# Performance work log

Measured on AMD Instinct MI355X. Metric: run time of the kernel, lower is better.

## Reference

```python
import jax, jax.numpy as jnp
import numpy as np

N, E, G = 20000, 50000, 64          # nodes, edges, graphs
IN_DIM, EDGE_DIM, H, OUT_DIM = 32, 16, 64, 6
EPS = 1e-5  # BatchNorm eps


def setup_inputs() -> dict:
    key = jax.random.key(0)
    ks = jax.random.split(key, 24)
    s = 0.05
    inp = {
        "x": jax.random.normal(ks[0], (N, IN_DIM), jnp.float32),
        "edge_attr": jax.random.normal(ks[1], (E, EDGE_DIM), jnp.float32),
        "src": jax.random.randint(ks[2], (E,), 0, N, jnp.int32),
        "dst": jax.random.randint(ks[3], (E,), 0, N, jnp.int32),
        "batch": jnp.sort(jax.random.randint(ks[4], (N,), 0, G, jnp.int32)),
        # node encoder
        "Wx": jax.random.normal(ks[5], (IN_DIM, H), jnp.float32) * s,
        "bx": jnp.zeros((H,), jnp.float32),
        # three edge MLPs: edge_dim -> H*H
        "We": jax.random.normal(ks[6], (3, EDGE_DIM, H * H), jnp.float32) * s,
        "be": jnp.zeros((3, H * H), jnp.float32),
        # NNConv root weights / biases
        "Wroot": jax.random.normal(ks[7], (3, H, H), jnp.float32) * s,
        "broot": jnp.zeros((3, H), jnp.float32),
        # BatchNorm (eval mode: running stats)
        "gamma": jnp.ones((3, H), jnp.float32),
        "beta": jnp.zeros((3, H), jnp.float32),
        "run_mean": jnp.zeros((3, H), jnp.float32),
        "run_var": jnp.ones((3, H), jnp.float32),
        # head
        "W1": jax.random.normal(ks[8], (H, H), jnp.float32) * s,
        "b1": jnp.zeros((H,), jnp.float32),
        "W2": jax.random.normal(ks[9], (H, OUT_DIM), jnp.float32) * s,
        "b2": jnp.zeros((OUT_DIM,), jnp.float32),
    }
    return inp


def _segment_mean(vals, idx, num_segments):
    tot = jax.ops.segment_sum(vals, idx, num_segments=num_segments)
    cnt = jax.ops.segment_sum(jnp.ones((vals.shape[0],), vals.dtype), idx,
                              num_segments=num_segments)
    return tot / jnp.maximum(cnt, 1.0)[:, None]


def reference(x, edge_attr, src, dst, batch, Wx, bx, We, be, Wroot, broot,
              gamma, beta, run_mean, run_var, W1, b1, W2, b2):
    h = x @ Wx + bx                                      # (N, H)
    for l in range(3):
        # per-edge H x H weight matrices from the edge MLP
        ew = jax.nn.relu(edge_attr @ We[l] + be[l]).reshape(-1, H, H)  # (E, H, H)
        msg = jnp.einsum('eh,eho->eo', h[src], ew)       # gather + per-edge matvec
        agg = _segment_mean(msg, dst, N)                 # scatter-mean at destinations
        out = agg + h @ Wroot[l] + broot[l]              # NNConv root + bias
        out = jax.nn.relu(out)
        # BatchNorm1d in eval mode (running stats); dropout is identity in eval
        out = gamma[l] * (out - run_mean[l]) * jax.lax.rsqrt(run_var[l] + EPS) + beta[l]
        h = out + h                                      # residual (shapes always match)
    pooled = _segment_mean(h, batch, G)                  # global_mean_pool -> (G, H)
    z = jax.nn.relu(pooled @ W1 + b1)
    return z @ W2 + b2                                   # (G, OUT_DIM)
```

## Files before the change

kernel.cpp:

```cpp
#include <hip/hip_runtime.h>
#include <hip/hip_bf16.h>

typedef _Float16 f16x2 __attribute__((ext_vector_type(2)));
typedef _Float16 f16x8 __attribute__((ext_vector_type(8)));
typedef float    f32x16 __attribute__((ext_vector_type(16)));

#define IN_DIM   32
#define EDGE_DIM 16
#define HDIM     64
#define OUT_DIM  6
#define BN_EPS   1e-5f

__global__ void k_zero(uint4* __restrict__ p, int n16) {
    int i = blockIdx.x * 256 + threadIdx.x;
    if (i < n16) p[i] = make_uint4(0u, 0u, 0u, 0u);
}

__global__ __launch_bounds__(256) void k_setup(
    const float* __restrict__ We, uint4* __restrict__ WeB,
    const float* __restrict__ x, const float* __restrict__ Wx,
    const float* __restrict__ bx, float* __restrict__ h,
    const float* __restrict__ ea, _Float16* __restrict__ eaH,
    const int* __restrict__ dstI, int* __restrict__ degI,
    const int* __restrict__ batch, int* __restrict__ start,
    int N, int E, int G, int PACKB, int ENCB, int PREPB)
{
    int bid = blockIdx.x;
    int t = threadIdx.x;
    if (bid < PACKB) {
        int tid = bid * 256 + t;
        int tile = tid >> 6, lane = tid & 63;
        int layer = tile >> 7;
        int r = tile & 127;
        int hh = r >> 1, oh = r & 1;
        int col = hh * 64 + oh * 32 + (lane & 31);
        int kbase = 8 * (lane >> 5);
        const float* base = We + (size_t)layer * 65536 + col;
        f16x8 v;
        #pragma unroll
        for (int j = 0; j < 8; ++j) v[j] = (_Float16)base[(size_t)(kbase + j) * 4096];
        WeB[(size_t)tile * 64 + lane] = __builtin_bit_cast(uint4, v);
        return;
    }
    bid -= PACKB;
    if (bid < ENCB) {
        int tid = bid * 256 + t;
        int n = tid >> 4, jq = tid & 15;
        if (n >= N) return;
        const float4* W4 = (const float4*)Wx;
        float4 acc = ((const float4*)bx)[jq];
        const float4* xv = (const float4*)(x + (size_t)n * IN_DIM);
        #pragma unroll
        for (int k4 = 0; k4 < 8; ++k4) {
            float4 xk = xv[k4];
            #pragma unroll
            for (int i = 0; i < 4; ++i) {
                float xs = (i == 0) ? xk.x : (i == 1) ? xk.y : (i == 2) ? xk.z : xk.w;
                float4 ww = W4[(k4 * 4 + i) * 16 + jq];
                acc.x += xs * ww.x; acc.y += xs * ww.y; acc.z += xs * ww.z; acc.w += xs * ww.w;
            }
        }
        ((float4*)h)[tid] = acc;
        return;
    }
    bid -= ENCB;
    if (bid < PREPB) {
        int tid = bid * 256 + t;
        int E8 = E * 8;
        if (tid < E8) {
            float2 v = ((const float2*)ea)[tid];
            f16x2 r; r[0] = (_Float16)v.x; r[1] = (_Float16)v.y;
            ((f16x2*)eaH)[tid] = r;
        }
        if (tid < E) atomicAdd(&degI[dstI[tid]], 1);
        return;
    }
    if (t <= G) {
        int lo = 0, hi = N;
        while (lo < hi) { int mid = (lo + hi) >> 1; if (batch[mid] < t) lo = mid + 1; else hi = mid; }
        start[t] = lo;
    }
}

__global__ __launch_bounds__(256, 4) void k_edge(
    const uint4* __restrict__ eaH4, const uint4* __restrict__ WeB,
    const float* __restrict__ be, const float* __restrict__ hin,
    const int* __restrict__ srcI, const int* __restrict__ dstI,
    float* __restrict__ agg, int E)
{
    __shared__ __align__(16) float hsT[64][68];
    __shared__ float beL[4096];
    const int t = threadIdx.x;
    const int l = t & 63;
    const int w = t >> 6;
    const int eb = blockIdx.x * 64;
    {
        const float4* bg = (const float4*)be;
        float4* bs = (float4*)beL;
        for (int i = t; i < 1024; i += 256) bs[i] = bg[i];
    }
    {
        int egc = min(eb + l, E - 1);
        int s = srcI[egc];
        const float4* hp = (const float4*)(hin + (size_t)s * HDIM + w * 16);
        float4 a = hp[0], b = hp[1], c = hp[2], d = hp[3];
        hsT[w*16+ 0][l] = a.x; hsT[w*16+ 1][l] = a.y; hsT[w*16+ 2][l] = a.z; hsT[w*16+ 3][l] = a.w;
        hsT[w*16+ 4][l] = b.x; hsT[w*16+ 5][l] = b.y; hsT[w*16+ 6][l] = b.z; hsT[w*16+ 7][l] = b.w;
        hsT[w*16+ 8][l] = c.x; hsT[w*16+ 9][l] = c.y; hsT[w*16+10][l] = c.z; hsT[w*16+11][l] = c.w;
        hsT[w*16+12][l] = d.x; hsT[w*16+13][l] = d.y; hsT[w*16+14][l] = d.z; hsT[w*16+15][l] = d.w;
    }
    __syncthreads();
    const int gp = w >> 1, oh = w & 1;
    const int ebw = eb + gp * 32, elw = gp * 32;
    const int row = l & 31, kg = l >> 5, obase = oh * 32;
    int ea_e = min(ebw + row, E - 1);
    f16x8 A = __builtin_bit_cast(f16x8, eaH4[(size_t)ea_e * 2 + kg]);
    float m[16];
    #pragma unroll
    for (int j = 0; j < 16; ++j) m[j] = 0.f;
    const uint4* Bb = WeB + (size_t)oh * 64 + l;
    uint4 Bv = Bb[0];
    for (int hh = 0; hh < 64; ++hh) {
        uint4 Bn;
        if (hh < 63) Bn = Bb[(size_t)(hh + 1) * 128];
        float bias = beL[hh * 64 + obase + row];
        f32x16 cin;
        #pragma unroll
        for (int j = 0; j < 16; ++j) cin[j] = bias;
        f32x16 z = __builtin_amdgcn_mfma_f32_32x32x16_f16(A, __builtin_bit_cast(f16x8, Bv), cin, 0, 0, 0);
        float4 q0 = *(const float4*)&hsT[hh][elw + 4 * kg + 0];
        float4 q1 = *(const float4*)&hsT[hh][elw + 4 * kg + 8];
        float4 q2 = *(const float4*)&hsT[hh][elw + 4 * kg + 16];
        float4 q3 = *(const float4*)&hsT[hh][elw + 4 * kg + 24];
        m[0]+=fmaxf(z[0],0.f)*q0.x;  m[1]+=fmaxf(z[1],0.f)*q0.y;
        m[2]+=fmaxf(z[2],0.f)*q0.z;  m[3]+=fmaxf(z[3],0.f)*q0.w;
        m[4]+=fmaxf(z[4],0.f)*q1.x;  m[5]+=fmaxf(z[5],0.f)*q1.y;
        m[6]+=fmaxf(z[6],0.f)*q1.z;  m[7]+=fmaxf(z[7],0.f)*q1.w;
        m[8]+=fmaxf(z[8],0.f)*q2.x;  m[9]+=fmaxf(z[9],0.f)*q2.y;
        m[10]+=fmaxf(z[10],0.f)*q2.z; m[11]+=fmaxf(z[11],0.f)*q2.w;
        m[12]+=fmaxf(z[12],0.f)*q3.x; m[13]+=fmaxf(z[13],0.f)*q3.y;
        m[14]+=fmaxf(z[14],0.f)*q3.z; m[15]+=fmaxf(z[15],0.f)*q3.w;
        Bv = Bn;
    }
    #pragma unroll
    for (int j = 0; j < 16; ++j) {
        int e = ebw + (j & 3) + 8 * (j >> 2) + 4 * kg;
        if (e < E) atomicAdd(&agg[(size_t)dstI[e] * HDIM + obase + row], m[j]);
    }
}

__global__ void k_update(
    float* __restrict__ agg, const int* __restrict__ degI,
    const float* __restrict__ hin, const float* __restrict__ Wroot,
    const float* __restrict__ broot, const float* __restrict__ gam,
    const float* __restrict__ bet, const float* __restrict__ rmean,
    const float* __restrict__ rvar, float* __restrict__ hout, int N)
{
    int tid = blockIdx.x * 256 + threadIdx.x;
    int n = tid >> 4, jq = tid & 15;
    if (n >= N) return;
    float dinv = 1.0f / fmaxf((float)degI[n], 1.0f);
    float4 acc = ((const float4*)broot)[jq];
    float4 ag = ((const float4*)agg)[tid];
    ((float4*)agg)[tid] = make_float4(0.f, 0.f, 0.f, 0.f);
    acc.x += ag.x * dinv; acc.y += ag.y * dinv; acc.z += ag.z * dinv; acc.w += ag.w * dinv;
    const float4* W4 = (const float4*)Wroot;
    const float4* hv = (const float4*)(hin + (size_t)n * HDIM);
    #pragma unroll
    for (int k4 = 0; k4 < 16; ++k4) {
        float4 hk = hv[k4];
        #pragma unroll
        for (int i = 0; i < 4; ++i) {
            float hsc = (i == 0) ? hk.x : (i == 1) ? hk.y : (i == 2) ? hk.z : hk.w;
            float4 ww = W4[(k4 * 4 + i) * 16 + jq];
            acc.x += hsc * ww.x; acc.y += hsc * ww.y; acc.z += hsc * ww.z; acc.w += hsc * ww.w;
        }
    }
    acc.x = fmaxf(acc.x, 0.f); acc.y = fmaxf(acc.y, 0.f);
    acc.z = fmaxf(acc.z, 0.f); acc.w = fmaxf(acc.w, 0.f);
    float4 g4 = ((const float4*)gam)[jq];
    float4 b4 = ((const float4*)bet)[jq];
    float4 mm4 = ((const float4*)rmean)[jq];
    float4 v4 = ((const float4*)rvar)[jq];
    float4 hres = ((const float4*)hin)[tid];
    float4 y;
    y.x = g4.x * (acc.x - mm4.x) * rsqrtf(v4.x + BN_EPS) + b4.x + hres.x;
    y.y = g4.y * (acc.y - mm4.y) * rsqrtf(v4.y + BN_EPS) + b4.y + hres.y;
    y.z = g4.z * (acc.z - mm4.z) * rsqrtf(v4.z + BN_EPS) + b4.z + hres.z;
    y.w = g4.w * (acc.w - mm4.w) * rsqrtf(v4.w + BN_EPS) + b4.w + hres.w;
    ((float4*)hout)[tid] = y;
}

__global__ __launch_bounds__(256) void k_pool_head(
    const float* __restrict__ h, const int* __restrict__ start,
    const float* __restrict__ W1, const float* __restrict__ b1,
    const float* __restrict__ W2, const float* __restrict__ b2,
    float* __restrict__ out)
{
    __shared__ float sums[16][68];
    __shared__ float pl[HDIM];
    __shared__ float zl[HDIM];
    int g = blockIdx.x;
    int s0 = start[g], s1 = start[g + 1];
    int t = threadIdx.x, jq = t & 15, rp = t >> 4;
    float4 acc = make_float4(0.f, 0.f, 0.f, 0.f);
    for (int n = s0 + rp; n < s1; n += 16) {
        float4 v = ((const float4*)h)[(size_t)n * 16 + jq];
        acc.x += v.x; acc.y += v.y; acc.z += v.z; acc.w += v.w;
    }
    *(float4*)&sums[rp][jq * 4] = acc;
    __syncthreads();
    if (t < HDIM) {
        float a = 0.f;
        #pragma unroll
        for (int r = 0; r < 16; ++r) a += sums[r][t];
        pl[t] = a / fmaxf((float)(s1 - s0), 1.0f);
    }
    __syncthreads();
    if (t < HDIM) {
        float a = b1[t];
        #pragma unroll
        for (int k = 0; k < HDIM; ++k) a += pl[k] * W1[k * HDIM + t];
        zl[t] = fmaxf(a, 0.f);
    }
    __syncthreads();
    if (t < OUT_DIM) {
        float a = b2[t];
        #pragma unroll
        for (int k = 0; k < HDIM; ++k) a += zl[k] * W2[k * OUT_DIM + t];
        out[(size_t)g * OUT_DIM + t] = a;
    }
}

extern "C" void kernel_launch(void* const* d_in, const int* in_sizes, int n_in,
                              void* d_out, int out_size, void* d_ws, size_t ws_size,
                              hipStream_t stream) {
    const float* x     = (const float*)d_in[0];
    const float* eattr = (const float*)d_in[1];
    const int*   src   = (const int*)d_in[2];
    const int*   dst   = (const int*)d_in[3];
    const int*   batch = (const int*)d_in[4];
    const float* Wx    = (const float*)d_in[5];
    const float* bx    = (const float*)d_in[6];
    const float* We    = (const float*)d_in[7];
    const float* be    = (const float*)d_in[8];
    const float* Wroot = (const float*)d_in[9];
    const float* broot = (const float*)d_in[10];
    const float* gam   = (const float*)d_in[11];
    const float* bet   = (const float*)d_in[12];
    const float* rmean = (const float*)d_in[13];
    const float* rvar  = (const float*)d_in[14];
    const float* W1    = (const float*)d_in[15];
    const float* b1    = (const float*)d_in[16];
    const float* W2    = (const float*)d_in[17];
    const float* b2    = (const float*)d_in[18];
    float* out = (float*)d_out;

    const int N = in_sizes[0] / IN_DIM;
    const int E = in_sizes[2];
    const int G = out_size / OUT_DIM;

    char* ws = (char*)d_ws;
    size_t off = 0;
    auto alloc = [&](size_t bytes) -> void* {
        void* p = ws + off;
        off = (off + bytes + 255) & ~(size_t)255;
        return p;
    };
    float*    h0    = (float*)alloc((size_t)N * HDIM * 4);
    float*    h1    = (float*)alloc((size_t)N * HDIM * 4);
    _Float16* eaH   = (_Float16*)alloc((size_t)E * 16 * 2);
    uint4*    WeB   = (uint4*)alloc((size_t)3 * 128 * 64 * 16);
    int*      start = (int*)alloc((size_t)(G + 1) * 4);
    size_t zoff = off;
    float*    agg   = (float*)alloc((size_t)N * HDIM * 4);
    int*      degI  = (int*)alloc((size_t)N * 4);
    size_t zbytes = off - zoff;
    (void)ws_size; (void)n_in;

    const int n16 = (int)(zbytes / 16);
    k_zero<<<(n16 + 255) / 256, 256, 0, stream>>>((uint4*)agg, n16);

    const int PACKB = 96;
    const int ENCB  = (N * 16 + 255) / 256;
    const int PREPB = (E * 8 + 255) / 256;
    k_setup<<<PACKB + ENCB + PREPB + 1, 256, 0, stream>>>(
        We, WeB, x, Wx, bx, h0, eattr, eaH, dst, degI, batch, start,
        N, E, G, PACKB, ENCB, PREPB);

    const float* hin = h0;
    float* hout = h1;
    const int edgeBlocks = (E + 63) / 64;
    for (int l = 0; l < 3; ++l) {
        k_edge<<<edgeBlocks, 256, 0, stream>>>(
            (const uint4*)eaH, WeB + (size_t)l * 8192, be + (size_t)l * 4096,
            hin, src, dst, agg, E);
        k_update<<<(N * 16 + 255) / 256, 256, 0, stream>>>(
            agg, degI, hin, Wroot + (size_t)l * 4096, broot + (size_t)l * 64,
            gam + (size_t)l * 64, bet + (size_t)l * 64, rmean + (size_t)l * 64,
            rvar + (size_t)l * 64, hout, N);
        float* tmp = hout; hout = (float*)hin; hin = tmp;
    }
    k_pool_head<<<G, 256, 0, stream>>>(hin, start, W1, b1, W2, b2, out);
}
```

Measured before the change: 211.9 us.

## Split edge kernel over hidden-dim halves and read transposed bias from global

Each edge block now handles only half of the 64 input-hidden rows, which doubles the grid and halves the per-block shared tile. The 16 KB per-block shared copy of the edge-MLP bias is dropped. A transposed bias array is built once in the setup kernel and read as float4 directly from global memory, with the bias added after the MFMA instead of preloaded into the accumulator. The hidden loop is unrolled by four with B prefetch and the occupancy hint is raised. Splitting the work doubles the atomic scatter traffic to agg and the A/src loads, in exchange for less shared memory and higher occupancy.

```diff
diff --git a/kernel.cpp b/kernel.cpp
--- a/kernel.cpp
+++ b/kernel.cpp
@@ -18,6 +18,7 @@
 
 __global__ __launch_bounds__(256) void k_setup(
     const float* __restrict__ We, uint4* __restrict__ WeB,
+    const float* __restrict__ be, float* __restrict__ beT,
     const float* __restrict__ x, const float* __restrict__ Wx,
     const float* __restrict__ bx, float* __restrict__ h,
     const float* __restrict__ ea, _Float16* __restrict__ eaH,
@@ -43,6 +44,14 @@
         return;
     }
     bid -= PACKB;
+    if (bid < 3) {
+        int layer = bid;
+        for (int i = t; i < 4096; i += 256) {
+            beT[(size_t)layer * 4096 + (i & 63) * 64 + (i >> 6)] = be[(size_t)layer * 4096 + i];
+        }
+        return;
+    }
+    bid -= 3;
     if (bid < ENCB) {
         int tid = bid * 256 + t;
         int n = tid >> 4, jq = tid & 15;
@@ -82,34 +91,31 @@
     }
 }
 
-__global__ __launch_bounds__(256, 4) void k_edge(
+__global__ __launch_bounds__(256, 6) void k_edge(
     const uint4* __restrict__ eaH4, const uint4* __restrict__ WeB,
-    const float* __restrict__ be, const float* __restrict__ hin,
+    const float* __restrict__ beT, const float* __restrict__ hin,
     const int* __restrict__ srcI, const int* __restrict__ dstI,
     float* __restrict__ agg, int E)
 {
-    __shared__ __align__(16) float hsT[64][68];
-    __shared__ float beL[4096];
+    __shared__ __align__(16) float hsT[32][68];
     const int t = threadIdx.x;
     const int l = t & 63;
     const int w = t >> 6;
-    const int eb = blockIdx.x * 64;
-    {
-        const float4* bg = (const float4*)be;
-        float4* bs = (float4*)beL;
-        for (int i = t; i < 1024; i += 256) bs[i] = bg[i];
-    }
+    const int eg = blockIdx.x >> 1;
+    const int hhalf = blockIdx.x & 1;
+    const int eb = eg * 64;
+    const int hbase = hhalf * 32;
+
     {
         int egc = min(eb + l, E - 1);
         int s = srcI[egc];
-        const float4* hp = (const float4*)(hin + (size_t)s * HDIM + w * 16);
-        float4 a = hp[0], b = hp[1], c = hp[2], d = hp[3];
-        hsT[w*16+ 0][l] = a.x; hsT[w*16+ 1][l] = a.y; hsT[w*16+ 2][l] = a.z; hsT[w*16+ 3][l] = a.w;
-        hsT[w*16+ 4][l] = b.x; hsT[w*16+ 5][l] = b.y; hsT[w*16+ 6][l] = b.z; hsT[w*16+ 7][l] = b.w;
-        hsT[w*16+ 8][l] = c.x; hsT[w*16+ 9][l] = c.y; hsT[w*16+10][l] = c.z; hsT[w*16+11][l] = c.w;
-        hsT[w*16+12][l] = d.x; hsT[w*16+13][l] = d.y; hsT[w*16+14][l] = d.z; hsT[w*16+15][l] = d.w;
+        const float4* hp = (const float4*)(hin + (size_t)s * HDIM + hbase + w * 8);
+        float4 a = hp[0], b = hp[1];
+        hsT[w*8+0][l] = a.x; hsT[w*8+1][l] = a.y; hsT[w*8+2][l] = a.z; hsT[w*8+3][l] = a.w;
+        hsT[w*8+4][l] = b.x; hsT[w*8+5][l] = b.y; hsT[w*8+6][l] = b.z; hsT[w*8+7][l] = b.w;
     }
     __syncthreads();
+
     const int gp = w >> 1, oh = w & 1;
     const int ebw = eb + gp * 32, elw = gp * 32;
     const int row = l & 31, kg = l >> 5, obase = oh * 32;
@@ -118,30 +124,54 @@
     float m[16];
     #pragma unroll
     for (int j = 0; j < 16; ++j) m[j] = 0.f;
+
+    const f32x16 zc = (f32x16)0.f;
     const uint4* Bb = WeB + (size_t)oh * 64 + l;
-    uint4 Bv = Bb[0];
-    for (int hh = 0; hh < 64; ++hh) {
-        uint4 Bn;
-        if (hh < 63) Bn = Bb[(size_t)(hh + 1) * 128];
-        float bias = beL[hh * 64 + obase + row];
-        f32x16 cin;
-        #pragma unroll
-        for (int j = 0; j < 16; ++j) cin[j] = bias;
-        f32x16 z = __builtin_amdgcn_mfma_f32_32x32x16_f16(A, __builtin_bit_cast(f16x8, Bv), cin, 0, 0, 0);
+    const float* beTb = beT + (size_t)(obase + row) * 64 + hbase;
+
+    auto step = [&](const uint4& Bv, int hh, float bias) {
+        f32x16 z = __builtin_amdgcn_mfma_f32_32x32x16_f16(
+            A, __builtin_bit_cast(f16x8, Bv), zc, 0, 0, 0);
         float4 q0 = *(const float4*)&hsT[hh][elw + 4 * kg + 0];
         float4 q1 = *(const float4*)&hsT[hh][elw + 4 * kg + 8];
         float4 q2 = *(const float4*)&hsT[hh][elw + 4 * kg + 16];
         float4 q3 = *(const float4*)&hsT[hh][elw + 4 * kg + 24];
-        m[0]+=fmaxf(z[0],0.f)*q0.x;  m[1]+=fmaxf(z[1],0.f)*q0.y;
-        m[2]+=fmaxf(z[2],0.f)*q0.z;  m[3]+=fmaxf(z[3],0.f)*q0.w;
-        m[4]+=fmaxf(z[4],0.f)*q1.x;  m[5]+=fmaxf(z[5],0.f)*q1.y;
-        m[6]+=fmaxf(z[6],0.f)*q1.z;  m[7]+=fmaxf(z[7],0.f)*q1.w;
-        m[8]+=fmaxf(z[8],0.f)*q2.x;  m[9]+=fmaxf(z[9],0.f)*q2.y;
-        m[10]+=fmaxf(z[10],0.f)*q2.z; m[11]+=fmaxf(z[11],0.f)*q2.w;
-        m[12]+=fmaxf(z[12],0.f)*q3.x; m[13]+=fmaxf(z[13],0.f)*q3.y;
-        m[14]+=fmaxf(z[14],0.f)*q3.z; m[15]+=fmaxf(z[15],0.f)*q3.w;
-        Bv = Bn;
-    }
+        m[0]  += fmaxf(z[0]  + bias, 0.f) * q0.x;
+        m[1]  += fmaxf(z[1]  + bias, 0.f) * q0.y;
+        m[2]  += fmaxf(z[2]  + bias, 0.f) * q0.z;
+        m[3]  += fmaxf(z[3]  + bias, 0.f) * q0.w;
+        m[4]  += fmaxf(z[4]  + bias, 0.f) * q1.x;
+        m[5]  += fmaxf(z[5]  + bias, 0.f) * q1.y;
+        m[6]  += fmaxf(z[6]  + bias, 0.f) * q1.z;
+        m[7]  += fmaxf(z[7]  + bias, 0.f) * q1.w;
+        m[8]  += fmaxf(z[8]  + bias, 0.f) * q2.x;
+        m[9]  += fmaxf(z[9]  + bias, 0.f) * q2.y;
+        m[10] += fmaxf(z[10] + bias, 0.f) * q2.z;
+        m[11] += fmaxf(z[11] + bias, 0.f) * q2.w;
+        m[12] += fmaxf(z[12] + bias, 0.f) * q3.x;
+        m[13] += fmaxf(z[13] + bias, 0.f) * q3.y;
+        m[14] += fmaxf(z[14] + bias, 0.f) * q3.z;
+        m[15] += fmaxf(z[15] + bias, 0.f) * q3.w;
+    };
+
+    uint4 B0 = Bb[(size_t)(hbase + 0) * 128];
+    uint4 B1 = Bb[(size_t)(hbase + 1) * 128];
+    uint4 B2 = Bb[(size_t)(hbase + 2) * 128];
+    uint4 B3 = Bb[(size_t)(hbase + 3) * 128];
+    #pragma unroll 1
+    for (int hh = 0; hh < 32; hh += 4) {
+        uint4 N0 = Bb[(size_t)(hbase + hh + 4) * 128];
+        uint4 N1 = Bb[(size_t)(hbase + hh + 5) * 128];
+        uint4 N2 = Bb[(size_t)(hbase + hh + 6) * 128];
+        uint4 N3 = Bb[(size_t)(hbase + hh + 7) * 128];
+        float4 bv = *(const float4*)(beTb + hh);
+        step(B0, hh + 0, bv.x);
+        step(B1, hh + 1, bv.y);
+        step(B2, hh + 2, bv.z);
+        step(B3, hh + 3, bv.w);
+        B0 = N0; B1 = N1; B2 = N2; B3 = N3;
+    }
+
     #pragma unroll
     for (int j = 0; j < 16; ++j) {
         int e = ebw + (j & 3) + 8 * (j >> 2) + 4 * kg;
@@ -270,7 +300,8 @@
     float*    h0    = (float*)alloc((size_t)N * HDIM * 4);
     float*    h1    = (float*)alloc((size_t)N * HDIM * 4);
     _Float16* eaH   = (_Float16*)alloc((size_t)E * 16 * 2);
-    uint4*    WeB   = (uint4*)alloc((size_t)3 * 128 * 64 * 16);
+    uint4*    WeB   = (uint4*)alloc((size_t)3 * 128 * 64 * 16 + 65536);
+    float*    beT   = (float*)alloc((size_t)3 * 4096 * 4);
     int*      start = (int*)alloc((size_t)(G + 1) * 4);
     size_t zoff = off;
     float*    agg   = (float*)alloc((size_t)N * HDIM * 4);
@@ -284,16 +315,16 @@
     const int PACKB = 96;
     const int ENCB  = (N * 16 + 255) / 256;
     const int PREPB = (E * 8 + 255) / 256;
-    k_setup<<<PACKB + ENCB + PREPB + 1, 256, 0, stream>>>(
-        We, WeB, x, Wx, bx, h0, eattr, eaH, dst, degI, batch, start,
+    k_setup<<<PACKB + 3 + ENCB + PREPB + 1, 256, 0, stream>>>(
+        We, WeB, be, beT, x, Wx, bx, h0, eattr, eaH, dst, degI, batch, start,
         N, E, G, PACKB, ENCB, PREPB);
 
     const float* hin = h0;
     float* hout = h1;
-    const int edgeBlocks = (E + 63) / 64;
+    const int edgeBlocks = ((E + 63) / 64) * 2;
     for (int l = 0; l < 3; ++l) {
         k_edge<<<edgeBlocks, 256, 0, stream>>>(
-            (const uint4*)eaH, WeB + (size_t)l * 8192, be + (size_t)l * 4096,
+            (const uint4*)eaH, WeB + (size_t)l * 8192, beT + (size_t)l * 4096,
             hin, src, dst, agg, E);
         k_update<<<(N * 16 + 255) / 256, 256, 0, stream>>>(
             agg, degI, hin, Wroot + (size_t)l * 4096, broot + (size_t)l * 64,
```

New measurement: 500.3 us. +136.1%, slower.

## Stream edge-MLP weights into LDS ring via async global_load_lds pipeline

Applied to the files above, without the earlier changes.

Replaces the register-prefetched per-iteration weight load in the edge kernel with a 4-slot per-wave LDS ring filled by asynchronous global-to-LDS loads, issued three iterations ahead and guarded by explicit vmcnt waits. The bias is now added after the MFMA instead of being broadcast into the accumulator input, and occupancy hint drops from 4 to 3 blocks per CU because of the extra LDS. The aim is to hide global weight-load latency behind MFMA work. In exchange it relies on manual waitcnt correctness, adds LDS traffic, and may reduce occupancy.

```diff
diff --git a/kernel.cpp b/kernel.cpp
--- a/kernel.cpp
+++ b/kernel.cpp
@@ -10,6 +10,9 @@
 #define HDIM     64
 #define OUT_DIM  6
 #define BN_EPS   1e-5f
+
+typedef __attribute__((address_space(1))) const void GASV;
+typedef __attribute__((address_space(3))) void LASV;
 
 __global__ void k_zero(uint4* __restrict__ p, int n16) {
     int i = blockIdx.x * 256 + threadIdx.x;
@@ -82,7 +85,7 @@
     }
 }
 
-__global__ __launch_bounds__(256, 4) void k_edge(
+__global__ __launch_bounds__(256, 3) void k_edge(
     const uint4* __restrict__ eaH4, const uint4* __restrict__ WeB,
     const float* __restrict__ be, const float* __restrict__ hin,
     const int* __restrict__ srcI, const int* __restrict__ dstI,
@@ -90,10 +93,12 @@
 {
     __shared__ __align__(16) float hsT[64][68];
     __shared__ float beL[4096];
+    __shared__ __align__(16) uint4 Bring[4][4][64];
     const int t = threadIdx.x;
     const int l = t & 63;
     const int w = t >> 6;
     const int eb = blockIdx.x * 64;
+
     {
         const float4* bg = (const float4*)be;
         float4* bs = (float4*)beL;
@@ -109,39 +114,58 @@
         hsT[w*16+ 8][l] = c.x; hsT[w*16+ 9][l] = c.y; hsT[w*16+10][l] = c.z; hsT[w*16+11][l] = c.w;
         hsT[w*16+12][l] = d.x; hsT[w*16+13][l] = d.y; hsT[w*16+14][l] = d.z; hsT[w*16+15][l] = d.w;
     }
-    __syncthreads();
     const int gp = w >> 1, oh = w & 1;
     const int ebw = eb + gp * 32, elw = gp * 32;
     const int row = l & 31, kg = l >> 5, obase = oh * 32;
+
+    const uint4* gsrc = WeB + (size_t)oh * 64 + l;
+    #pragma unroll
+    for (int s = 0; s < 3; ++s) {
+        __builtin_amdgcn_global_load_lds((GASV*)(gsrc + (size_t)s * 128),
+                                         (LASV*)&Bring[w][s][0], 16, 0, 0);
+    }
+    __syncthreads();
+
     int ea_e = min(ebw + row, E - 1);
     f16x8 A = __builtin_bit_cast(f16x8, eaH4[(size_t)ea_e * 2 + kg]);
     float m[16];
     #pragma unroll
     for (int j = 0; j < 16; ++j) m[j] = 0.f;
-    const uint4* Bb = WeB + (size_t)oh * 64 + l;
-    uint4 Bv = Bb[0];
+    const f32x16 zc = (f32x16)0.f;
+
+    #pragma unroll 1
     for (int hh = 0; hh < 64; ++hh) {
-        uint4 Bn;
-        if (hh < 63) Bn = Bb[(size_t)(hh + 1) * 128];
+        asm volatile("s_waitcnt vmcnt(2)" ::: "memory");
+        __builtin_amdgcn_sched_barrier(0);
+        uint4 Bv = Bring[w][hh & 3][l];
         float bias = beL[hh * 64 + obase + row];
-        f32x16 cin;
-        #pragma unroll
-        for (int j = 0; j < 16; ++j) cin[j] = bias;
-        f32x16 z = __builtin_amdgcn_mfma_f32_32x32x16_f16(A, __builtin_bit_cast(f16x8, Bv), cin, 0, 0, 0);
+        f32x16 z = __builtin_amdgcn_mfma_f32_32x32x16_f16(
+            A, __builtin_bit_cast(f16x8, Bv), zc, 0, 0, 0);
+        int hn = (hh + 3) & 63;
+        __builtin_amdgcn_global_load_lds((GASV*)(gsrc + (size_t)hn * 128),
+                                         (LASV*)&Bring[w][hn & 3][0], 16, 0, 0);
         float4 q0 = *(const float4*)&hsT[hh][elw + 4 * kg + 0];
         float4 q1 = *(const float4*)&hsT[hh][elw + 4 * kg + 8];
         float4 q2 = *(const float4*)&hsT[hh][elw + 4 * kg + 16];
         float4 q3 = *(const float4*)&hsT[hh][elw + 4 * kg + 24];
-        m[0]+=fmaxf(z[0],0.f)*q0.x;  m[1]+=fmaxf(z[1],0.f)*q0.y;
-        m[2]+=fmaxf(z[2],0.f)*q0.z;  m[3]+=fmaxf(z[3],0.f)*q0.w;
-        m[4]+=fmaxf(z[4],0.f)*q1.x;  m[5]+=fmaxf(z[5],0.f)*q1.y;
-        m[6]+=fmaxf(z[6],0.f)*q1.z;  m[7]+=fmaxf(z[7],0.f)*q1.w;
-        m[8]+=fmaxf(z[8],0.f)*q2.x;  m[9]+=fmaxf(z[9],0.f)*q2.y;
-        m[10]+=fmaxf(z[10],0.f)*q2.z; m[11]+=fmaxf(z[11],0.f)*q2.w;
-        m[12]+=fmaxf(z[12],0.f)*q3.x; m[13]+=fmaxf(z[13],0.f)*q3.y;
-        m[14]+=fmaxf(z[14],0.f)*q3.z; m[15]+=fmaxf(z[15],0.f)*q3.w;
-        Bv = Bn;
-    }
+        m[0]  += fmaxf(z[0]  + bias, 0.f) * q0.x;
+        m[1]  += fmaxf(z[1]  + bias, 0.f) * q0.y;
+        m[2]  += fmaxf(z[2]  + bias, 0.f) * q0.z;
+        m[3]  += fmaxf(z[3]  + bias, 0.f) * q0.w;
+        m[4]  += fmaxf(z[4]  + bias, 0.f) * q1.x;
+        m[5]  += fmaxf(z[5]  + bias, 0.f) * q1.y;
+        m[6]  += fmaxf(z[6]  + bias, 0.f) * q1.z;
+        m[7]  += fmaxf(z[7]  + bias, 0.f) * q1.w;
+        m[8]  += fmaxf(z[8]  + bias, 0.f) * q2.x;
+        m[9]  += fmaxf(z[9]  + bias, 0.f) * q2.y;
+        m[10] += fmaxf(z[10] + bias, 0.f) * q2.z;
+        m[11] += fmaxf(z[11] + bias, 0.f) * q2.w;
+        m[12] += fmaxf(z[12] + bias, 0.f) * q3.x;
+        m[13] += fmaxf(z[13] + bias, 0.f) * q3.y;
+        m[14] += fmaxf(z[14] + bias, 0.f) * q3.z;
+        m[15] += fmaxf(z[15] + bias, 0.f) * q3.w;
+    }
+
     #pragma unroll
     for (int j = 0; j < 16; ++j) {
         int e = ebw + (j & 3) + 8 * (j >> 2) + 4 * kg;
```

New measurement: 224.6 us. 6.0% more time.
